# Optimization experiments

Measured on AMD Instinct MI355X. Metric: run time of the kernel, lower is better.

## Reference

```python
import jax, jax.numpy as jnp
import numpy as np

H = 4096
V = 32000
BT = 2048
IGNORE_INDEX = -100
WEIGHT_HARD = 0.5
WEIGHT_SOFT = 0.5
EPS = 1e-12  # F.normalize eps


def setup_inputs() -> dict:
    key = jax.random.key(0)
    k0, k1, k2, k3, k4 = jax.random.split(key, 5)
    student = jax.random.normal(k0, (BT, H // 2), dtype=jnp.float32)
    teacher = jax.random.normal(k1, (BT, H), dtype=jnp.float32)
    W_student = jax.random.normal(k2, (V, H // 2), dtype=jnp.float32) * (1.0 / np.sqrt(H // 2))
    W_teacher = jax.random.normal(k3, (V, H), dtype=jnp.float32) * (1.0 / np.sqrt(H))
    target = jax.random.randint(k4, (BT,), 0, V, dtype=jnp.int64)
    return {"student": student, "W_student": W_student, "teacher": teacher,
            "W_teacher": W_teacher, "target": target}


def reference(student, W_student, teacher, W_teacher, target):
    # Fused linear projections to vocab space
    s_logits = jnp.einsum("bh,vh->bv", student, W_student)   # [BT, V]
    t_logits = jnp.einsum("bh,vh->bv", teacher, W_teacher)   # [BT, V]

    n = target.shape[0]
    valid = target != IGNORE_INDEX                            # [BT]

    # Hard loss: cross-entropy(student_logits, target), sum over valid / BT
    logp = jax.nn.log_softmax(s_logits, axis=-1)
    safe_tgt = jnp.where(valid, target, 0)
    nll = -jnp.take_along_axis(logp, safe_tgt[:, None], axis=-1)[:, 0]
    hard_loss = jnp.sum(jnp.where(valid, nll, 0.0)) / n

    # Soft loss: 1 - cosine_similarity(student_logits, teacher_logits) per row
    s_norm = jnp.maximum(jnp.linalg.norm(s_logits, axis=-1, keepdims=True), EPS)
    t_norm = jnp.maximum(jnp.linalg.norm(t_logits, axis=-1, keepdims=True), EPS)
    cos = jnp.sum((s_logits / s_norm) * (t_logits / t_norm), axis=-1)  # [BT]
    soft_loss = jnp.sum(1.0 - cos) / n

    return WEIGHT_HARD * hard_loss + WEIGHT_SOFT * soft_loss
```

## Files before the change

kernel.cpp:

```cpp
#include <hip/hip_runtime.h>
#include <hip/hip_bf16.h>

#define H2 2048
#define HT 4096
#define NV 32000
#define NBT 2048
#define BM 128
#define BN 128
#define BK 32
#define LDT 40
#define NVB (NV / BN)

typedef __attribute__((ext_vector_type(8))) short short8;
typedef __attribute__((ext_vector_type(8))) unsigned short ushort8;
typedef __attribute__((ext_vector_type(4))) float floatx4;

static __device__ __forceinline__ unsigned int pk_bf16(float a, float b) {
  __hip_bfloat162 h = __float22bfloat162_rn(make_float2(a, b));
  union { __hip_bfloat162 h; unsigned int u; } c;
  c.h = h;
  return c.u;
}

static __device__ __forceinline__ void gload_lds16(const void* g, void* l) {
  __builtin_amdgcn_global_load_lds(
      (const __attribute__((address_space(1))) unsigned int*)g,
      (__attribute__((address_space(3))) unsigned int*)l, 16, 0, 0);
}

__global__ void cvt_bf16_kernel(const float* __restrict__ src,
                                unsigned int* __restrict__ dst, int n) {
  int i = blockIdx.x * blockDim.x + threadIdx.x;
  int base = i * 8;
  if (base >= n) return;
  float4 f0 = *(const float4*)(src + base);
  float4 f1 = *(const float4*)(src + base + 4);
  uint4 o;
  o.x = pk_bf16(f0.x, f0.y);
  o.y = pk_bf16(f0.z, f0.w);
  o.z = pk_bf16(f1.x, f1.y);
  o.w = pk_bf16(f1.z, f1.w);
  *(uint4*)(dst + i * 4) = o;
}


template <int K>
static __device__ __forceinline__ void gemm_phase(
    const unsigned short* __restrict__ act,
    const unsigned short* __restrict__ w,
    int row0, int col0, int tid,
    unsigned short* sA, unsigned short* sB,
    int abase, int bbase, floatx4 (&acc)[4][4])
{
  const int r0 = tid >> 2;
  const int c0 = (tid & 3) * 8;
  const unsigned short* a0 = act + (size_t)(row0 + r0) * K + c0;
  const unsigned short* a1 = act + (size_t)(row0 + r0 + 64) * K + c0;
  const unsigned short* b0 = w + (size_t)(col0 + r0) * K + c0;
  const unsigned short* b1 = w + (size_t)(col0 + r0 + 64) * K + c0;
  unsigned short* lA0 = sA + tid * 8;
  unsigned short* lA1 = sA + (256 + tid) * 8;
  unsigned short* lB0 = sB + tid * 8;
  unsigned short* lB1 = sB + (256 + tid) * 8;

#pragma unroll 1
  for (int k0 = 0; k0 < K; k0 += BK) {
    __syncthreads();
    gload_lds16(a0, lA0);
    gload_lds16(a1, lA1);
    gload_lds16(b0, lB0);
    gload_lds16(b1, lB1);
    a0 += BK; a1 += BK; b0 += BK; b1 += BK;
    __syncthreads();
    short8 af[4], bf[4];
#pragma unroll
    for (int i = 0; i < 4; ++i)
      af[i] = *(const short8*)(sA + abase + i * 16 * BK);
#pragma unroll
    for (int j = 0; j < 4; ++j)
      bf[j] = *(const short8*)(sB + bbase + j * 16 * BK);
#pragma unroll
    for (int i = 0; i < 4; ++i)
#pragma unroll
      for (int j = 0; j < 4; ++j)
        acc[i][j] = __builtin_amdgcn_mfma_f32_16x16x32_bf16(
            af[i], bf[j], acc[i][j], 0, 0, 0);
  }
}

__global__ __launch_bounds__(256, 2) void fused_gemm_lds_kernel(
    const unsigned short* __restrict__ sbf,
    const unsigned short* __restrict__ tbf,
    const unsigned short* __restrict__ Wsb,
    const unsigned short* __restrict__ Wtb,
    const int* __restrict__ target,
    float* __restrict__ part,
    float* __restrict__ s_tgt_out)
{
  __shared__ unsigned short sA[BM * BK];
  __shared__ unsigned short sB[BN * BK];
  __shared__ float sRed[BM][4];
  __shared__ int sTgt[BM];

  const int tid = threadIdx.x;
  const int row0 = blockIdx.x * BM;
  const int col0 = blockIdx.y * BN;
  const int lane = tid & 63;
  const int wv = tid >> 6;
  const int wr = wv >> 1;
  const int wc = wv & 1;

  if (tid < BM) {
    sTgt[tid] = target[row0 + tid];
    sRed[tid][0] = 0.f; sRed[tid][1] = 0.f;
    sRed[tid][2] = 0.f; sRed[tid][3] = 0.f;
  }

  floatx4 acc_s[4][4];
  floatx4 acc_t[4][4];
#pragma unroll
  for (int i = 0; i < 4; ++i)
#pragma unroll
    for (int j = 0; j < 4; ++j) {
      acc_s[i][j] = (floatx4){0.f, 0.f, 0.f, 0.f};
      acc_t[i][j] = (floatx4){0.f, 0.f, 0.f, 0.f};
    }

  const int mrow = lane & 15;
  const int koff = (lane >> 4) * 8;
  const int abase = (wr * 64 + mrow) * BK + koff;
  const int bbase = (wc * 64 + mrow) * BK + koff;

  gemm_phase<H2>(sbf, Wsb, row0, col0, tid, sA, sB, abase, bbase, acc_s);
  gemm_phase<HT>(tbf, Wtb, row0, col0, tid, sA, sB, abase, bbase, acc_t);

#pragma unroll
  for (int i = 0; i < 4; ++i) {
#pragma unroll
    for (int r = 0; r < 4; ++r) {
      const int row_l = wr * 64 + i * 16 + (lane >> 4) * 4 + r;
      float e = 0.f, dp = 0.f, ss = 0.f, tt = 0.f;
#pragma unroll
      for (int j = 0; j < 4; ++j) {
        float s = acc_s[i][j][r];
        float t = acc_t[i][j][r];
        e += __expf(s);
        dp += s * t;
        ss += s * s;
        tt += t * t;
        const int col_l = wc * 64 + j * 16 + (lane & 15);
        if (sTgt[row_l] == col0 + col_l) s_tgt_out[row0 + row_l] = s;
      }
#pragma unroll
      for (int off = 1; off < 16; off <<= 1) {
        e  += __shfl_xor(e,  off, 16);
        dp += __shfl_xor(dp, off, 16);
        ss += __shfl_xor(ss, off, 16);
        tt += __shfl_xor(tt, off, 16);
      }
      if ((lane & 15) == 0) {
        atomicAdd(&sRed[row_l][0], e);
        atomicAdd(&sRed[row_l][1], dp);
        atomicAdd(&sRed[row_l][2], ss);
        atomicAdd(&sRed[row_l][3], tt);
      }
    }
  }
  __syncthreads();
  if (tid < BM) {
    float* p = part + (size_t)blockIdx.y * 4 * NBT + row0 + tid;
    p[0]       = sRed[tid][0];
    p[NBT]     = sRed[tid][1];
    p[2 * NBT] = sRed[tid][2];
    p[3 * NBT] = sRed[tid][3];
  }
}


__global__ __launch_bounds__(256, 2) void fused_gemm_kernel(
    const unsigned short* __restrict__ sbf,
    const unsigned short* __restrict__ tbf,
    const float* __restrict__ Ws,
    const float* __restrict__ Wt,
    const int* __restrict__ target,
    float* __restrict__ part,
    float* __restrict__ s_tgt_out)
{
  __shared__ unsigned short sA[BM * LDT];
  __shared__ unsigned short sB[BN * LDT];
  __shared__ float sRed[BM][4];
  __shared__ int sTgt[BM];

  const int tid = threadIdx.x;
  const int row0 = blockIdx.x * BM;
  const int col0 = blockIdx.y * BN;
  const int lane = tid & 63;
  const int wv = tid >> 6;
  const int wr = wv >> 1;
  const int wc = wv & 1;

  if (tid < BM) {
    sTgt[tid] = target[row0 + tid];
    sRed[tid][0] = 0.f; sRed[tid][1] = 0.f;
    sRed[tid][2] = 0.f; sRed[tid][3] = 0.f;
  }

  floatx4 acc_s[4][4];
  floatx4 acc_t[4][4];
#pragma unroll
  for (int i = 0; i < 4; ++i)
#pragma unroll
    for (int j = 0; j < 4; ++j) {
      acc_s[i][j] = (floatx4){0.f, 0.f, 0.f, 0.f};
      acc_t[i][j] = (floatx4){0.f, 0.f, 0.f, 0.f};
    }

  const int sr = tid >> 1;
  const int sk = (tid & 1) << 4;
  const int mrow = lane & 15;
  const int koff = (lane >> 4) << 3;
  const int abase = (wr * 64 + mrow) * LDT + koff;
  const int bbase = (wc * 64 + mrow) * LDT + koff;

  {
    const unsigned short* ap = sbf + (size_t)(row0 + sr) * H2 + sk;
    const float* bp = Ws + (size_t)(col0 + sr) * H2 + sk;
#pragma unroll 1
    for (int k0 = 0; k0 < H2; k0 += BK) {
      ushort8 a0 = *(const ushort8*)(ap);
      ushort8 a1 = *(const ushort8*)(ap + 8);
      float4 b0 = *(const float4*)(bp);
      float4 b1 = *(const float4*)(bp + 4);
      float4 b2 = *(const float4*)(bp + 8);
      float4 b3 = *(const float4*)(bp + 12);
      ap += BK; bp += BK;
      __syncthreads();
      *(ushort8*)(&sA[sr * LDT + sk]) = a0;
      *(ushort8*)(&sA[sr * LDT + sk + 8]) = a1;
      uint4 u0, u1;
      u0.x = pk_bf16(b0.x, b0.y); u0.y = pk_bf16(b0.z, b0.w);
      u0.z = pk_bf16(b1.x, b1.y); u0.w = pk_bf16(b1.z, b1.w);
      u1.x = pk_bf16(b2.x, b2.y); u1.y = pk_bf16(b2.z, b2.w);
      u1.z = pk_bf16(b3.x, b3.y); u1.w = pk_bf16(b3.z, b3.w);
      *(uint4*)(&sB[sr * LDT + sk]) = u0;
      *(uint4*)(&sB[sr * LDT + sk + 8]) = u1;
      __syncthreads();
      short8 af[4], bfrag[4];
#pragma unroll
      for (int i = 0; i < 4; ++i)
        af[i] = *(const short8*)(&sA[abase + i * 16 * LDT]);
#pragma unroll
      for (int j = 0; j < 4; ++j)
        bfrag[j] = *(const short8*)(&sB[bbase + j * 16 * LDT]);
#pragma unroll
      for (int i = 0; i < 4; ++i)
#pragma unroll
        for (int j = 0; j < 4; ++j)
          acc_s[i][j] = __builtin_amdgcn_mfma_f32_16x16x32_bf16(
              af[i], bfrag[j], acc_s[i][j], 0, 0, 0);
    }
  }
  {
    const unsigned short* ap = tbf + (size_t)(row0 + sr) * HT + sk;
    const float* bp = Wt + (size_t)(col0 + sr) * HT + sk;
#pragma unroll 1
    for (int k0 = 0; k0 < HT; k0 += BK) {
      ushort8 a0 = *(const ushort8*)(ap);
      ushort8 a1 = *(const ushort8*)(ap + 8);
      float4 b0 = *(const float4*)(bp);
      float4 b1 = *(const float4*)(bp + 4);
      float4 b2 = *(const float4*)(bp + 8);
      float4 b3 = *(const float4*)(bp + 12);
      ap += BK; bp += BK;
      __syncthreads();
      *(ushort8*)(&sA[sr * LDT + sk]) = a0;
      *(ushort8*)(&sA[sr * LDT + sk + 8]) = a1;
      uint4 u0, u1;
      u0.x = pk_bf16(b0.x, b0.y); u0.y = pk_bf16(b0.z, b0.w);
      u0.z = pk_bf16(b1.x, b1.y); u0.w = pk_bf16(b1.z, b1.w);
      u1.x = pk_bf16(b2.x, b2.y); u1.y = pk_bf16(b2.z, b2.w);
      u1.z = pk_bf16(b3.x, b3.y); u1.w = pk_bf16(b3.z, b3.w);
      *(uint4*)(&sB[sr * LDT + sk]) = u0;
      *(uint4*)(&sB[sr * LDT + sk + 8]) = u1;
      __syncthreads();
      short8 af[4], bfrag[4];
#pragma unroll
      for (int i = 0; i < 4; ++i)
        af[i] = *(const short8*)(&sA[abase + i * 16 * LDT]);
#pragma unroll
      for (int j = 0; j < 4; ++j)
        bfrag[j] = *(const short8*)(&sB[bbase + j * 16 * LDT]);
#pragma unroll
      for (int i = 0; i < 4; ++i)
#pragma unroll
        for (int j = 0; j < 4; ++j)
          acc_t[i][j] = __builtin_amdgcn_mfma_f32_16x16x32_bf16(
              af[i], bfrag[j], acc_t[i][j], 0, 0, 0);
    }
  }

#pragma unroll
  for (int i = 0; i < 4; ++i) {
#pragma unroll
    for (int r = 0; r < 4; ++r) {
      const int row_l = wr * 64 + i * 16 + (lane >> 4) * 4 + r;
      float e = 0.f, dp = 0.f, ss = 0.f, tt = 0.f;
#pragma unroll
      for (int j = 0; j < 4; ++j) {
        float s = acc_s[i][j][r];
        float t = acc_t[i][j][r];
        e += __expf(s);
        dp += s * t;
        ss += s * s;
        tt += t * t;
        const int col_l = wc * 64 + j * 16 + (lane & 15);
        if (sTgt[row_l] == col0 + col_l) s_tgt_out[row0 + row_l] = s;
      }
#pragma unroll
      for (int off = 1; off < 16; off <<= 1) {
        e  += __shfl_xor(e,  off, 16);
        dp += __shfl_xor(dp, off, 16);
        ss += __shfl_xor(ss, off, 16);
        tt += __shfl_xor(tt, off, 16);
      }
      if ((lane & 15) == 0) {
        atomicAdd(&sRed[row_l][0], e);
        atomicAdd(&sRed[row_l][1], dp);
        atomicAdd(&sRed[row_l][2], ss);
        atomicAdd(&sRed[row_l][3], tt);
      }
    }
  }
  __syncthreads();
  if (tid < BM) {
    float* p = part + (size_t)blockIdx.y * 4 * NBT + row0 + tid;
    p[0]       = sRed[tid][0];
    p[NBT]     = sRed[tid][1];
    p[2 * NBT] = sRed[tid][2];
    p[3 * NBT] = sRed[tid][3];
  }
}


__global__ void row_loss_kernel(const float* __restrict__ part,
                                const float* __restrict__ s_tgt,
                                const int* __restrict__ target,
                                float* __restrict__ row_loss) {
  const int row = blockIdx.x * blockDim.x + threadIdx.x;
  if (row >= NBT) return;
  float e = 0.f, dp = 0.f, ss = 0.f, tt = 0.f;
  for (int v = 0; v < NVB; ++v) {
    const float* p = part + (size_t)v * 4 * NBT + row;
    e  += p[0];
    dp += p[NBT];
    ss += p[2 * NBT];
    tt += p[3 * NBT];
  }
  const float lse = logf(e);
  const int tg = target[row];
  const float st = s_tgt[row];
  const float nll = (tg != -100) ? (lse - st) : 0.f;
  const float ns = fmaxf(sqrtf(ss), 1e-12f);
  const float nt = fmaxf(sqrtf(tt), 1e-12f);
  const float c = dp / (ns * nt);
  row_loss[row] = (0.5f * nll + 0.5f * (1.f - c)) * (1.f / (float)NBT);
}

__global__ void final_reduce_kernel(const float* __restrict__ row_loss,
                                    float* __restrict__ out) {
  __shared__ float sm[4];
  float v = 0.f;
  for (int i = threadIdx.x; i < NBT; i += 256) v += row_loss[i];
#pragma unroll
  for (int off = 32; off >= 1; off >>= 1) v += __shfl_down(v, off, 64);
  if ((threadIdx.x & 63) == 0) sm[threadIdx.x >> 6] = v;
  __syncthreads();
  if (threadIdx.x == 0) out[0] = sm[0] + sm[1] + sm[2] + sm[3];
}

extern "C" void kernel_launch(void* const* d_in, const int* in_sizes, int n_in,
                              void* d_out, int out_size, void* d_ws, size_t ws_size,
                              hipStream_t stream) {
  const float* student = (const float*)d_in[0];
  const float* Ws      = (const float*)d_in[1];
  const float* teacher = (const float*)d_in[2];
  const float* Wt      = (const float*)d_in[3];
  const int*   target  = (const int*)d_in[4];

  const size_t nS  = (size_t)NBT * H2;
  const size_t nT  = (size_t)NBT * HT;
  const size_t nWs = (size_t)NV * H2;
  const size_t nWt = (size_t)NV * HT;
  const size_t nPart = (size_t)NVB * 4 * NBT;

  const size_t ws_needed_big =
      (nS + nT + nWs + nWt) * 2 + (nPart + 2 * NBT) * 4;

  if (ws_size >= ws_needed_big) {
    unsigned short* sbf = (unsigned short*)d_ws;
    unsigned short* tbf = sbf + nS;
    unsigned short* Wsb = tbf + nT;
    unsigned short* Wtb = Wsb + nWs;
    float* part     = (float*)(Wtb + nWt);
    float* s_tgt    = part + nPart;
    float* row_loss = s_tgt + NBT;

    cvt_bf16_kernel<<<(int)(nS / 8 / 256), 256, 0, stream>>>(
        student, (unsigned int*)sbf, (int)nS);
    cvt_bf16_kernel<<<(int)(nT / 8 / 256), 256, 0, stream>>>(
        teacher, (unsigned int*)tbf, (int)nT);
    cvt_bf16_kernel<<<(int)(nWs / 8 / 256), 256, 0, stream>>>(
        Ws, (unsigned int*)Wsb, (int)nWs);
    cvt_bf16_kernel<<<(int)(nWt / 8 / 256), 256, 0, stream>>>(
        Wt, (unsigned int*)Wtb, (int)nWt);

    dim3 grid(NBT / BM, NV / BN);
    fused_gemm_lds_kernel<<<grid, 256, 0, stream>>>(
        sbf, tbf, Wsb, Wtb, target, part, s_tgt);

    row_loss_kernel<<<NBT / 256, 256, 0, stream>>>(part, s_tgt, target, row_loss);
    final_reduce_kernel<<<1, 256, 0, stream>>>(row_loss, (float*)d_out);
  } else {
    unsigned short* sbf = (unsigned short*)d_ws;
    unsigned short* tbf = sbf + nS;
    float* part     = (float*)(tbf + nT);
    float* s_tgt    = part + nPart;
    float* row_loss = s_tgt + NBT;

    cvt_bf16_kernel<<<(int)(nS / 8 / 256), 256, 0, stream>>>(
        student, (unsigned int*)sbf, (int)nS);
    cvt_bf16_kernel<<<(int)(nT / 8 / 256), 256, 0, stream>>>(
        teacher, (unsigned int*)tbf, (int)nT);

    dim3 grid(NBT / BM, NV / BN);
    fused_gemm_kernel<<<grid, 256, 0, stream>>>(sbf, tbf, Ws, Wt, target,
                                                part, s_tgt);

    row_loss_kernel<<<NBT / 256, 256, 0, stream>>>(part, s_tgt, target, row_loss);
    final_reduce_kernel<<<1, 256, 0, stream>>>(row_loss, (float*)d_out);
  }
}
```

Measured before the change: 1.997 ms.

## Double-buffer LDS GEMM with larger 128x256x64 tiles, swizzle, and block remap

Replaces the single-buffered 128x128x32 bf16 MFMA GEMM with a 512-thread kernel using 128x256 tiles, BK=64 and two LDS stages. Global-to-LDS loads for the next stage overlap MFMA work, synchronized by explicit waitcnt and barriers. XOR swizzling cuts LDS bank conflicts, and a block-index remap groups blocks for L2 reuse. s_setprio raises priority during MFMA. The cost is more LDS (about 96KB) per block, which may limit occupancy, and the hand-tuned wait counts must be correct.

```diff
diff --git a/kernel.cpp b/kernel.cpp
--- a/kernel.cpp
+++ b/kernel.cpp
@@ -5,6 +5,12 @@
 #define HT 4096
 #define NV 32000
 #define NBT 2048
+
+#define BM2 128
+#define BN2 256
+#define BK2 64
+#define NVB2 (NV / BN2)
+
 #define BM 128
 #define BN 128
 #define BK 32
@@ -45,50 +51,90 @@
 
 
 template <int K>
-static __device__ __forceinline__ void gemm_phase(
+static __device__ __forceinline__ void gemm_pipe(
     const unsigned short* __restrict__ act,
     const unsigned short* __restrict__ w,
-    int row0, int col0, int tid,
-    unsigned short* sA, unsigned short* sB,
-    int abase, int bbase, floatx4 (&acc)[4][4])
+    const int row0, const int col0, const int tid,
+    const int aoff, const int boff,
+    unsigned short (*__restrict__ sA)[BM2 * BK2],
+    unsigned short (*__restrict__ sB)[BN2 * BK2],
+    floatx4 (&acc)[4][4])
 {
-  const int r0 = tid >> 2;
-  const int c0 = (tid & 3) * 8;
-  const unsigned short* a0 = act + (size_t)(row0 + r0) * K + c0;
-  const unsigned short* a1 = act + (size_t)(row0 + r0 + 64) * K + c0;
-  const unsigned short* b0 = w + (size_t)(col0 + r0) * K + c0;
-  const unsigned short* b1 = w + (size_t)(col0 + r0 + 64) * K + c0;
-  unsigned short* lA0 = sA + tid * 8;
-  unsigned short* lA1 = sA + (256 + tid) * 8;
-  unsigned short* lB0 = sB + tid * 8;
-  unsigned short* lB1 = sB + (256 + tid) * 8;
+  constexpr int NT = K / BK2;
+  const int r8 = tid >> 3;
+  const int usw = ((tid & 7) ^ (r8 & 7)) * 8;
+
+  const unsigned short* pa0 = act + (size_t)(row0 + r8) * K + usw;
+  const unsigned short* pa1 = pa0 + (size_t)64 * K;
+  const unsigned short* pb0 = w + (size_t)(col0 + r8) * K + usw;
+  const unsigned short* pb1 = pb0 + (size_t)64 * K;
+  const unsigned short* pb2 = pb0 + (size_t)128 * K;
+  const unsigned short* pb3 = pb0 + (size_t)192 * K;
+
+#define STAGE6(buf)                                   \
+  do {                                                \
+    gload_lds16(pa0, &sA[buf][tid * 8]);              \
+    gload_lds16(pa1, &sA[buf][4096 + tid * 8]);       \
+    gload_lds16(pb0, &sB[buf][tid * 8]);              \
+    gload_lds16(pb1, &sB[buf][4096 + tid * 8]);       \
+    gload_lds16(pb2, &sB[buf][8192 + tid * 8]);       \
+    gload_lds16(pb3, &sB[buf][12288 + tid * 8]);      \
+    pa0 += BK2; pa1 += BK2;                           \
+    pb0 += BK2; pb1 += BK2; pb2 += BK2; pb3 += BK2;   \
+  } while (0)
+
+  STAGE6(0);
+  STAGE6(1);
+  asm volatile("s_waitcnt vmcnt(6)" ::: "memory");
+  __builtin_amdgcn_s_barrier();
 
 #pragma unroll 1
-  for (int k0 = 0; k0 < K; k0 += BK) {
-    __syncthreads();
-    gload_lds16(a0, lA0);
-    gload_lds16(a1, lA1);
-    gload_lds16(b0, lB0);
-    gload_lds16(b1, lB1);
-    a0 += BK; a1 += BK; b0 += BK; b1 += BK;
-    __syncthreads();
-    short8 af[4], bf[4];
-#pragma unroll
-    for (int i = 0; i < 4; ++i)
-      af[i] = *(const short8*)(sA + abase + i * 16 * BK);
-#pragma unroll
-    for (int j = 0; j < 4; ++j)
-      bf[j] = *(const short8*)(sB + bbase + j * 16 * BK);
+  for (int t = 0; t < NT; ++t) {
+    const int cur = t & 1;
+    const unsigned short* sAc = sA[cur];
+    const unsigned short* sBc = sB[cur];
+
+    short8 a0[4], a1[4], b0[4], b1[4];
+#pragma unroll
+    for (int i = 0; i < 4; ++i) {
+      a0[i] = *(const short8*)(sAc + (aoff + i * 1024));
+      a1[i] = *(const short8*)(sAc + ((aoff ^ 32) + i * 1024));
+    }
+#pragma unroll
+    for (int j = 0; j < 4; ++j) {
+      b0[j] = *(const short8*)(sBc + (boff + j * 1024));
+      b1[j] = *(const short8*)(sBc + ((boff ^ 32) + j * 1024));
+    }
+    asm volatile("s_waitcnt lgkmcnt(0)" ::: "memory");
+    __builtin_amdgcn_s_barrier();
+
+    if (t + 2 < NT) {
+      STAGE6(cur);
+      asm volatile("s_waitcnt vmcnt(6)" ::: "memory");
+    } else if (t + 1 < NT) {
+      asm volatile("s_waitcnt vmcnt(0)" ::: "memory");
+    }
+    __builtin_amdgcn_s_barrier();
+
+    __builtin_amdgcn_s_setprio(1);
 #pragma unroll
     for (int i = 0; i < 4; ++i)
 #pragma unroll
       for (int j = 0; j < 4; ++j)
         acc[i][j] = __builtin_amdgcn_mfma_f32_16x16x32_bf16(
-            af[i], bf[j], acc[i][j], 0, 0, 0);
-  }
-}
-
-__global__ __launch_bounds__(256, 2) void fused_gemm_lds_kernel(
+            a0[i], b0[j], acc[i][j], 0, 0, 0);
+#pragma unroll
+    for (int i = 0; i < 4; ++i)
+#pragma unroll
+      for (int j = 0; j < 4; ++j)
+        acc[i][j] = __builtin_amdgcn_mfma_f32_16x16x32_bf16(
+            a1[i], b1[j], acc[i][j], 0, 0, 0);
+    __builtin_amdgcn_s_setprio(0);
+  }
+#undef STAGE6
+}
+
+__global__ __launch_bounds__(512, 2) void fused_gemm_pipe_kernel(
     const unsigned short* __restrict__ sbf,
     const unsigned short* __restrict__ tbf,
     const unsigned short* __restrict__ Wsb,
@@ -97,25 +143,35 @@
     float* __restrict__ part,
     float* __restrict__ s_tgt_out)
 {
-  __shared__ unsigned short sA[BM * BK];
-  __shared__ unsigned short sB[BN * BK];
-  __shared__ float sRed[BM][4];
-  __shared__ int sTgt[BM];
+  __shared__ unsigned short sA[2][BM2 * BK2];
+  __shared__ unsigned short sB[2][BN2 * BK2];
+  __shared__ float sRed[BM2][4];
+  __shared__ int sTgt[BM2];
 
   const int tid = threadIdx.x;
-  const int row0 = blockIdx.x * BM;
-  const int col0 = blockIdx.y * BN;
-  const int lane = tid & 63;
-  const int wv = tid >> 6;
-  const int wr = wv >> 1;
-  const int wc = wv & 1;
-
-  if (tid < BM) {
+
+  const int lin = blockIdx.x + (int)gridDim.x * blockIdx.y;
+  const int swz = (lin & 7) * 250 + (lin >> 3);
+  const int bx = swz & 15;
+  const int by = swz >> 4;
+  const int row0 = bx * BM2;
+  const int col0 = by * BN2;
+
+  if (tid < BM2) {
     sTgt[tid] = target[row0 + tid];
     sRed[tid][0] = 0.f; sRed[tid][1] = 0.f;
     sRed[tid][2] = 0.f; sRed[tid][3] = 0.f;
   }
 
+  const int lane = tid & 63;
+  const int wv = tid >> 6;
+  const int wr = wv >> 2;
+  const int wc = wv & 3;
+  const int ku = lane >> 4;
+  const int u0 = (ku ^ (lane & 7)) * 8;
+  const int aoff = (wr * 64 + (lane & 15)) * BK2 + u0;
+  const int boff = (wc * 64 + (lane & 15)) * BK2 + u0;
+
   floatx4 acc_s[4][4];
   floatx4 acc_t[4][4];
 #pragma unroll
@@ -126,13 +182,8 @@
       acc_t[i][j] = (floatx4){0.f, 0.f, 0.f, 0.f};
     }
 
-  const int mrow = lane & 15;
-  const int koff = (lane >> 4) * 8;
-  const int abase = (wr * 64 + mrow) * BK + koff;
-  const int bbase = (wc * 64 + mrow) * BK + koff;
-
-  gemm_phase<H2>(sbf, Wsb, row0, col0, tid, sA, sB, abase, bbase, acc_s);
-  gemm_phase<HT>(tbf, Wtb, row0, col0, tid, sA, sB, abase, bbase, acc_t);
+  gemm_pipe<H2>(sbf, Wsb, row0, col0, tid, aoff, boff, sA, sB, acc_s);
+  gemm_pipe<HT>(tbf, Wtb, row0, col0, tid, aoff, boff, sA, sB, acc_t);
 
 #pragma unroll
   for (int i = 0; i < 4; ++i) {
@@ -167,8 +218,8 @@
     }
   }
   __syncthreads();
-  if (tid < BM) {
-    float* p = part + (size_t)blockIdx.y * 4 * NBT + row0 + tid;
+  if (tid < BM2) {
+    float* p = part + (size_t)by * 4 * NBT + row0 + tid;
     p[0]       = sRed[tid][0];
     p[NBT]     = sRed[tid][1];
     p[2 * NBT] = sRed[tid][2];
@@ -345,11 +396,11 @@
 __global__ void row_loss_kernel(const float* __restrict__ part,
                                 const float* __restrict__ s_tgt,
                                 const int* __restrict__ target,
-                                float* __restrict__ row_loss) {
+                                float* __restrict__ row_loss, int nvb) {
   const int row = blockIdx.x * blockDim.x + threadIdx.x;
   if (row >= NBT) return;
   float e = 0.f, dp = 0.f, ss = 0.f, tt = 0.f;
-  for (int v = 0; v < NVB; ++v) {
+  for (int v = 0; v < nvb; ++v) {
     const float* p = part + (size_t)v * 4 * NBT + row;
     e  += p[0];
     dp += p[NBT];
@@ -391,10 +442,11 @@
   const size_t nT  = (size_t)NBT * HT;
   const size_t nWs = (size_t)NV * H2;
   const size_t nWt = (size_t)NV * HT;
-  const size_t nPart = (size_t)NVB * 4 * NBT;
+  const size_t nPart2 = (size_t)NVB2 * 4 * NBT;
+  const size_t nPart  = (size_t)NVB * 4 * NBT;
 
   const size_t ws_needed_big =
-      (nS + nT + nWs + nWt) * 2 + (nPart + 2 * NBT) * 4;
+      (nS + nT + nWs + nWt) * 2 + (nPart2 + 2 * NBT) * 4;
 
   if (ws_size >= ws_needed_big) {
     unsigned short* sbf = (unsigned short*)d_ws;
@@ -402,7 +454,7 @@
     unsigned short* Wsb = tbf + nT;
     unsigned short* Wtb = Wsb + nWs;
     float* part     = (float*)(Wtb + nWt);
-    float* s_tgt    = part + nPart;
+    float* s_tgt    = part + nPart2;
     float* row_loss = s_tgt + NBT;
 
     cvt_bf16_kernel<<<(int)(nS / 8 / 256), 256, 0, stream>>>(
@@ -414,11 +466,12 @@
     cvt_bf16_kernel<<<(int)(nWt / 8 / 256), 256, 0, stream>>>(
         Wt, (unsigned int*)Wtb, (int)nWt);
 
-    dim3 grid(NBT / BM, NV / BN);
-    fused_gemm_lds_kernel<<<grid, 256, 0, stream>>>(
+    dim3 grid(NBT / BM2, NV / BN2);
+    fused_gemm_pipe_kernel<<<grid, 512, 0, stream>>>(
         sbf, tbf, Wsb, Wtb, target, part, s_tgt);
 
-    row_loss_kernel<<<NBT / 256, 256, 0, stream>>>(part, s_tgt, target, row_loss);
+    row_loss_kernel<<<NBT / 256, 256, 0, stream>>>(part, s_tgt, target,
+                                                   row_loss, NVB2);
     final_reduce_kernel<<<1, 256, 0, stream>>>(row_loss, (float*)d_out);
   } else {
     unsigned short* sbf = (unsigned short*)d_ws;
@@ -436,7 +489,8 @@
     fused_gemm_kernel<<<grid, 256, 0, stream>>>(sbf, tbf, Ws, Wt, target,
                                                 part, s_tgt);
 
-    row_loss_kernel<<<NBT / 256, 256, 0, stream>>>(part, s_tgt, target, row_loss);
+    row_loss_kernel<<<NBT / 256, 256, 0, stream>>>(part, s_tgt, target,
+                                                   row_loss, NVB);
     final_reduce_kernel<<<1, 256, 0, stream>>>(row_loss, (float*)d_out);
   }
 }
```

Measured after the change: 1.986 ms. About the same (-0.5%).
